# Optimization experiments

Hardware: AMD Instinct MI355X
Metric: run time of the kernel (lower is better)

The kernel has to match this reference:

```python
import jax, jax.numpy as jnp
import numpy as np

J, F_ = 17, 32  # joints x per-joint features; C = J*F_ = 544
H = 8           # num_heads
EPS = 1e-5


def _layernorm(x, g, b):
    mu = jnp.mean(x, axis=-1, keepdims=True)
    var = jnp.mean((x - mu) ** 2, axis=-1, keepdims=True)
    return (x - mu) * jax.lax.rsqrt(var + EPS) * g + b


def setup_inputs() -> dict:
    key = jax.random.key(0)
    ks = jax.random.split(key, 8)
    B, N, C = 8, 1024, J * F_
    x = jax.random.normal(ks[0], (B, N, C), dtype=jnp.float32)
    s = 1.0 / np.sqrt(C)
    return {
        "x": x,
        "norm_g": jnp.ones((F_,), jnp.float32),
        "norm_b": jnp.zeros((F_,), jnp.float32),
        "ap_w": jax.random.normal(ks[1], (1, F_), jnp.float32) / np.sqrt(F_),
        "ap_b": jnp.zeros((1,), jnp.float32),
        "norm2_g": jnp.ones((C,), jnp.float32),
        "norm2_b": jnp.zeros((C,), jnp.float32),
        "qkv_w": jax.random.normal(ks[2], (3 * C, C), jnp.float32) * s,
        "proj_w": jax.random.normal(ks[3], (C, C), jnp.float32) * s,
        "proj_b": jnp.zeros((C,), jnp.float32),
        "scaling_factor": jnp.array([2.0], jnp.float32),
    }


def reference(x, norm_g, norm_b, ap_w, ap_b, norm2_g, norm2_b, qkv_w, proj_w, proj_b, scaling_factor):
    B, N, C = x.shape
    hd = C // H
    # --- attention pooling over joints ---
    xr = x.reshape(B, N, J, F_)
    xr = _layernorm(xr, norm_g, norm_b)                      # [B,N,17,32]
    scores = jnp.einsum('bnjf,of->bnjo', xr, ap_w)[..., 0] + ap_b[0]  # [B,N,17]
    # nn.Softmax(dim=1): softmax over sequence axis N (faithful to source)
    w = jax.nn.softmax(scores, axis=1)
    xp = (xr * w[..., None]).reshape(B, N, C)
    xp = _layernorm(xp, norm2_g, norm2_b)
    # --- position-scaled self-attention ---
    positions = jnp.linspace(0.0, 1.0, N, dtype=jnp.float32)  # [N]
    pos_scale = jnp.exp(-scaling_factor[0] * (positions - 0.5) ** 2)  # per-key scale
    qkv = (xp @ qkv_w.T).reshape(B, N, 3, H, hd)
    q = qkv[:, :, 0].transpose(0, 2, 1, 3)  # [B,H,N,hd]
    k = qkv[:, :, 1].transpose(0, 2, 1, 3)
    v = qkv[:, :, 2].transpose(0, 2, 1, 3)
    scale = hd ** -0.5
    attn = jnp.einsum('bhqd,bhkd->bhqk', q, k) * (scale * pos_scale[None, None, None, :])
    attn = jax.nn.softmax(attn, axis=-1)
    out = jnp.einsum('bhqk,bhkd->bhqd', attn, v)
    out = out.transpose(0, 2, 1, 3).reshape(B, N, C)
    return out @ proj_w.T + proj_b
```

## Files before the change

kernel.cpp:

```cpp
#include <hip/hip_runtime.h>
#include <hip/hip_bf16.h>

#define BB 8
#define NN 1024
#define CC 544
#define JJ 17
#define FF 32
#define HH 8
#define HD 68
#define BN 8192
#define KD 544
#define NCQ 1632
#define NCQP 1664
#define NCPP 640
#define NKB 9
#define BHSZ 73728
#define AQR 64

using f32x4  = __attribute__((ext_vector_type(4))) float;
using bf16x8 = __attribute__((ext_vector_type(8))) short;

__device__ __forceinline__ void gld_lds16(const void* g, void* l) {
  __builtin_amdgcn_global_load_lds(
      (const __attribute__((address_space(1))) void*)g,
      (__attribute__((address_space(3))) void*)l, 16, 0, 0);
}

__global__ __launch_bounds__(256) void wconv(const float* __restrict__ qkv_w,
                                             const float* __restrict__ proj_w,
                                             __hip_bfloat16* __restrict__ qw,
                                             __hip_bfloat16* __restrict__ pw,
                                             char* __restrict__ qkp) {
  int bid = blockIdx.x, t = threadIdx.x;
  if (bid < NCQP + NCPP) {
    bool isq = bid < NCQP;
    int r = isq ? bid : bid - NCQP;
    const float* src = isq ? qkv_w : proj_w;
    __hip_bfloat16* dst = isq ? qw : pw;
    int nrows = isq ? NCQ : CC;
    if (t < KD / 4) {
      int c = t * 4;
      float4 v;
      if (r < nrows) v = *(const float4*)(src + (size_t)r * KD + c);
      else           v = float4{0.f, 0.f, 0.f, 0.f};
      __hip_bfloat16 o[4] = {__float2bfloat16(v.x), __float2bfloat16(v.y),
                             __float2bfloat16(v.z), __float2bfloat16(v.w)};
      *(unsigned long long*)(dst + (size_t)r * KD + c) = *(unsigned long long*)o;
    }
  } else {
    int row = (bid - (NCQP + NCPP)) * 256 + t;
    if (row < 131072) {
      int bhT = row >> 10, n = row & 1023;
      char* p = qkp + (size_t)bhT * 147456 + 131072 + (size_t)n * 16 + 8;
      *(unsigned long long*)p = 0ull;
    }
  }
}

__global__ __launch_bounds__(256) void ln1_scores(const float* __restrict__ x,
                                                  const float* __restrict__ g,
                                                  const float* __restrict__ bta,
                                                  const float* __restrict__ apw,
                                                  const float* __restrict__ apb,
                                                  __hip_bfloat16* __restrict__ xr,
                                                  float* __restrict__ scores) {
  int wv = threadIdx.x >> 6, lane = threadIdx.x & 63;
  int bn = blockIdx.x * 4 + wv;
  int f = lane & 31, half = lane >> 5;
  const float* row = x + (size_t)bn * CC;
  float gg = g[f], bb = bta[f], aw = apw[f], ab = apb[0];
  for (int it = 0; it < 9; ++it) {
    int j = it * 2 + half;
    bool act = (j < JJ);
    float v = act ? row[j * FF + f] : 0.f;
    float s = v;
    for (int m = 16; m >= 1; m >>= 1) s += __shfl_xor(s, m);
    float mu = s * (1.f / 32.f);
    float dv = v - mu;
    float s2 = dv * dv;
    for (int m = 16; m >= 1; m >>= 1) s2 += __shfl_xor(s2, m);
    float xn = dv * rsqrtf(s2 * (1.f / 32.f) + 1e-5f) * gg + bb;
    float sc = xn * aw;
    for (int m = 16; m >= 1; m >>= 1) sc += __shfl_xor(sc, m);
    if (act) {
      xr[(size_t)bn * CC + j * FF + f] = __float2bfloat16(xn);
      if (f == 0) scores[bn * JJ + j] = sc + ab;
    }
  }
}

__global__ __launch_bounds__(256) void softmax_red(const float* __restrict__ scores,
                                                   float2* __restrict__ tab) {
  int bj = blockIdx.x;
  int b = bj / JJ, j = bj - b * JJ;
  const float* s = scores + (size_t)b * NN * JJ + j;
  int t = threadIdx.x;
  float v[4];
  float mx = -1e30f;
#pragma unroll
  for (int i = 0; i < 4; ++i) { v[i] = s[(t + 256 * i) * JJ]; mx = fmaxf(mx, v[i]); }
#pragma unroll
  for (int m = 32; m >= 1; m >>= 1) mx = fmaxf(mx, __shfl_xor(mx, m));
  __shared__ float red[4];
  if ((t & 63) == 0) red[t >> 6] = mx;
  __syncthreads();
  mx = fmaxf(fmaxf(red[0], red[1]), fmaxf(red[2], red[3]));
  float sum = 0.f;
#pragma unroll
  for (int i = 0; i < 4; ++i) sum += __expf(v[i] - mx);
#pragma unroll
  for (int m = 32; m >= 1; m >>= 1) sum += __shfl_xor(sum, m);
  __shared__ float red2[4];
  if ((t & 63) == 0) red2[t >> 6] = sum;
  __syncthreads();
  if (t == 0) {
    sum = red2[0] + red2[1] + red2[2] + red2[3];
    tab[bj] = make_float2(mx, 1.f / sum);
  }
}

__global__ __launch_bounds__(256) void ln2_xp(const __hip_bfloat16* __restrict__ xr,
                                              const float* __restrict__ scores,
                                              const float2* __restrict__ tab,
                                              const float* __restrict__ g2,
                                              const float* __restrict__ b2,
                                              __hip_bfloat16* __restrict__ xp) {
  __shared__ float wsh[4][JJ];
  int wv = threadIdx.x >> 6, lane = threadIdx.x & 63;
  int bn = blockIdx.x * 4 + wv;
  if (lane < JJ) {
    float sc = scores[bn * JJ + lane];
    float2 mi = tab[(bn >> 10) * JJ + lane];
    wsh[wv][lane] = __expf(sc - mi.x) * mi.y;
  }
  float vals[9];
  float sum = 0.f;
  for (int it = 0; it < 9; ++it) {
    int c = it * 64 + lane;
    float v = 0.f;
    if (c < CC) v = __bfloat162float(xr[(size_t)bn * CC + c]) * wsh[wv][c >> 5];
    vals[it] = v;
    sum += v;
  }
  for (int m = 32; m >= 1; m >>= 1) sum += __shfl_xor(sum, m);
  float mu = sum * (1.f / 544.f);
  float s2 = 0.f;
  for (int it = 0; it < 9; ++it) {
    int c = it * 64 + lane;
    if (c < CC) { float dv = vals[it] - mu; s2 += dv * dv; }
  }
  for (int m = 32; m >= 1; m >>= 1) s2 += __shfl_xor(s2, m);
  float rstd = rsqrtf(s2 * (1.f / 544.f) + 1e-5f);
  for (int it = 0; it < 9; ++it) {
    int c = it * 64 + lane;
    if (c < CC)
      xp[(size_t)bn * CC + c] = __float2bfloat16((vals[it] - mu) * rstd * g2[c] + b2[c]);
  }
}

template <int MODE>
__global__ __launch_bounds__(256) void gemm_nt(const __hip_bfloat16* __restrict__ A,
                                               const __hip_bfloat16* __restrict__ Bw,
                                               __hip_bfloat16* __restrict__ Qp,
                                               __hip_bfloat16* __restrict__ Kp,
                                               __hip_bfloat16* __restrict__ Vt,
                                               float* __restrict__ Cf,
                                               const float* __restrict__ bias,
                                               const float* __restrict__ sfp) {
  __shared__ __hip_bfloat16 As[2][128 * 32];
  __shared__ __hip_bfloat16 Bs[2][128 * 32];
  const int t = threadIdx.x;
  const int w = t >> 6, lane = t & 63;
  const int fr = lane & 15, fq = lane >> 4;
  const int bi = blockIdx.x;
  const int xcd = bi & 7, j = bi >> 3;
  const int bx = xcd * 8 + (j & 7), by = j >> 3;
  const int m0 = bx * 128;
  const int n0 = by * 128;
  const int wm = (w >> 1) * 64, wn = (w & 1) * 64;

  f32x4 acc[4][4] = {};

  const __hip_bfloat16* Ag = A + (size_t)m0 * KD;
  const __hip_bfloat16* Bg = Bw + (size_t)n0 * KD;

#pragma unroll
  for (int i2 = 0; i2 < 2; ++i2) {
    int cb = (i2 * 4 + w) * 64;
    int chunk = cb + lane;
    int row = chunk >> 2, c16 = chunk & 3;
    gld_lds16(Ag + (size_t)row * KD + c16 * 8, &As[0][cb * 8]);
    gld_lds16(Bg + (size_t)row * KD + c16 * 8, &Bs[0][cb * 8]);
  }
  __syncthreads();

  for (int kt = 0; kt < 17; ++kt) {
    const int cur = kt & 1;
    if (kt < 16) {
      const int k0 = (kt + 1) * 32;
#pragma unroll
      for (int i2 = 0; i2 < 2; ++i2) {
        int cb = (i2 * 4 + w) * 64;
        int chunk = cb + lane;
        int row = chunk >> 2, c16 = chunk & 3;
        gld_lds16(Ag + (size_t)row * KD + k0 + c16 * 8, &As[1 - cur][cb * 8]);
        gld_lds16(Bg + (size_t)row * KD + k0 + c16 * 8, &Bs[1 - cur][cb * 8]);
      }
    }
    bf16x8 af[4], bfr[4];
#pragma unroll
    for (int tm = 0; tm < 4; ++tm)
      af[tm] = *(const bf16x8*)&As[cur][(wm + tm * 16 + fr) * 32 + fq * 8];
#pragma unroll
    for (int tn = 0; tn < 4; ++tn)
      bfr[tn] = *(const bf16x8*)&Bs[cur][(wn + tn * 16 + fr) * 32 + fq * 8];
#pragma unroll
    for (int tm = 0; tm < 4; ++tm)
#pragma unroll
      for (int tn = 0; tn < 4; ++tn)
        acc[tm][tn] = __builtin_amdgcn_mfma_f32_16x16x32_bf16(af[tm], bfr[tn], acc[tm][tn], 0, 0, 0);
    __syncthreads();
  }

  if (MODE == 1) {
#pragma unroll
    for (int tn = 0; tn < 4; ++tn) {
      int o = n0 + wn + tn * 16 + fr;
      if (o < CC) {
        float bb = bias[o];
#pragma unroll
        for (int tm = 0; tm < 4; ++tm) {
          int m = m0 + wm + tm * 16 + fq * 4;
#pragma unroll
          for (int r = 0; r < 4; ++r)
            Cf[(size_t)(m + r) * CC + o] = acc[tm][tn][r] + bb;
        }
      }
    }
  } else {
    int b = m0 >> 10;
    float sf = sfp[0];
#pragma unroll
    for (int tn = 0; tn < 4; ++tn) {
      int o = n0 + wn + tn * 16 + fr;
      if (o < 2 * CC) {
        bool is_k = (o >= CC);
        int oo = is_k ? o - CC : o;
        int h = oo / HD;
        int d = oo - h * HD;
        __hip_bfloat16* base = is_k ? Kp : Qp;
        __hip_bfloat16* dst = base + (size_t)(b * HH + h) * BHSZ + (d >> 3) * (NN * 8) + (d & 7);
#pragma unroll
        for (int tm = 0; tm < 4; ++tm) {
          int m = m0 + wm + tm * 16 + fq * 4;
          int n = m & (NN - 1);
#pragma unroll
          for (int r = 0; r < 4; ++r) {
            float v = acc[tm][tn][r];
            if (is_k) {
              float pos = (n + r) * (1.f / 1023.f) - 0.5f;
              v *= __expf(-sf * pos * pos) * (0.12126781251816650f * 1.44269504088896340f);
            }
            dst[(size_t)(n + r) * 8] = __float2bfloat16(v);
          }
        }
      } else if (o < NCQ) {
        int oo = o - 2 * CC;
        int h = oo / HD;
        int d = oo - h * HD;
        __hip_bfloat16* vrow = Vt + (((size_t)b * HH + h) * HD + d) * NN;
#pragma unroll
        for (int tm = 0; tm < 4; ++tm) {
          int m = m0 + wm + tm * 16 + fq * 4;
          int n = m & (NN - 1);
#pragma unroll
          for (int r = 0; r < 4; ++r)
            vrow[n + r] = __float2bfloat16(acc[tm][tn][r]);
        }
      }
    }
  }
}

__global__ __launch_bounds__(128) void attn_kernel(const __hip_bfloat16* __restrict__ Qp,
                                                   const __hip_bfloat16* __restrict__ Kp,
                                                   const __hip_bfloat16* __restrict__ Vt,
                                                   __hip_bfloat16* __restrict__ Ao) {
  __shared__ __hip_bfloat16 Qs[NKB * 64 * 8];
  __shared__ __hip_bfloat16 Ks[2][NKB * 64 * 8];
  __shared__ __hip_bfloat16 Zs[64 * 8];
  const int t = threadIdx.x;
  const int w = t >> 6, lane = t & 63;
  const int fr = lane & 15, fq = lane >> 4;
  const int idx = blockIdx.x;
  const int bh = idx & 63, qt = idx >> 6;
  const int h = bh & 7, b = bh >> 3;

  const __hip_bfloat16* qtile = Qp + (size_t)bh * BHSZ + (size_t)qt * AQR * 8;
  const __hip_bfloat16* kbase = Kp + (size_t)bh * BHSZ;
  const __hip_bfloat16* vbase = Vt + (size_t)bh * HD * NN;

  *(unsigned long long*)&Zs[t * 4] = 0ull;
#pragma unroll
  for (int i = 0; i < 5; ++i) {
    int kb = i * 2 + w;
    if (kb < NKB) gld_lds16(qtile + (size_t)kb * (NN * 8) + lane * 8, &Qs[kb * 64 * 8]);
  }
#pragma unroll
  for (int i = 0; i < 5; ++i) {
    int kb = i * 2 + w;
    if (kb < NKB) gld_lds16(kbase + (size_t)kb * (NN * 8) + lane * 8, &Ks[0][kb * 64 * 8]);
  }
  __syncthreads();
  bf16x8 qa[2][3];
#pragma unroll
  for (int ks = 0; ks < 3; ++ks) {
    const __hip_bfloat16* qb = (ks < 2 || fq == 0) ? &Qs[(ks * 4 + fq) * 64 * 8] : Zs;
#pragma unroll
    for (int g = 0; g < 2; ++g)
      qa[g][ks] = *(const bf16x8*)&qb[(w * 32 + g * 16 + fr) * 8];
  }
  __syncthreads();

  f32x4 o_acc[2][5] = {};
  float l_part[2][4] = {};
  const int dclamp = (fr < 4) ? 0 : 1;

  for (int kt = 0; kt < 16; ++kt) {
    const int cur = kt & 1;
    bf16x8 vfrag[5][2];
#pragma unroll
    for (int tv = 0; tv < 5; ++tv) {
      int d = tv * 16 + fr;
      int dc = (tv == 4 && dclamp) ? 0 : d;
#pragma unroll
      for (int ks2 = 0; ks2 < 2; ++ks2)
        vfrag[tv][ks2] = *(const bf16x8*)(vbase + (size_t)dc * NN + kt * 64 + ks2 * 32 + fq * 8);
    }
    if (kt < 15) {
      const __hip_bfloat16* ktile = kbase + (size_t)(kt + 1) * 64 * 8;
#pragma unroll
      for (int i = 0; i < 5; ++i) {
        int kb = i * 2 + w;
        if (kb < NKB) gld_lds16(ktile + (size_t)kb * (NN * 8) + lane * 8, &Ks[1 - cur][kb * 64 * 8]);
      }
    }

    f32x4 s[2][4] = {};
#pragma unroll
    for (int ks = 0; ks < 3; ++ks) {
      const __hip_bfloat16* kbL = (ks < 2 || fq == 0) ? &Ks[cur][(ks * 4 + fq) * 64 * 8] : Zs;
#pragma unroll
      for (int tn = 0; tn < 4; ++tn) {
        bf16x8 kb = *(const bf16x8*)&kbL[(tn * 16 + fr) * 8];
        s[0][tn] = __builtin_amdgcn_mfma_f32_16x16x32_bf16(qa[0][ks], kb, s[0][tn], 0, 0, 0);
        s[1][tn] = __builtin_amdgcn_mfma_f32_16x16x32_bf16(qa[1][ks], kb, s[1][tn], 0, 0, 0);
      }
    }
#pragma unroll
    for (int g = 0; g < 2; ++g) {
      __hip_bfloat16* Pw = &Qs[(w * 2 + g) * 1152];
#pragma unroll
      for (int tn = 0; tn < 4; ++tn)
#pragma unroll
        for (int r = 0; r < 4; ++r) {
          float p = __builtin_amdgcn_exp2f(s[g][tn][r]);
          l_part[g][r] += p;
          Pw[(fq * 4 + r) * 72 + tn * 16 + fr] = __float2bfloat16(p);
        }
    }
#pragma unroll
    for (int ks2 = 0; ks2 < 2; ++ks2) {
      bf16x8 pa0 = *(const bf16x8*)&Qs[(w * 2 + 0) * 1152 + fr * 72 + ks2 * 32 + fq * 8];
      bf16x8 pa1 = *(const bf16x8*)&Qs[(w * 2 + 1) * 1152 + fr * 72 + ks2 * 32 + fq * 8];
#pragma unroll
      for (int tv = 0; tv < 5; ++tv) {
        o_acc[0][tv] = __builtin_amdgcn_mfma_f32_16x16x32_bf16(pa0, vfrag[tv][ks2], o_acc[0][tv], 0, 0, 0);
        o_acc[1][tv] = __builtin_amdgcn_mfma_f32_16x16x32_bf16(pa1, vfrag[tv][ks2], o_acc[1][tv], 0, 0, 0);
      }
    }
    __syncthreads();
  }
#pragma unroll
  for (int g = 0; g < 2; ++g) {
    __hip_bfloat16* obase = Ao + (size_t)(b * NN + qt * AQR + w * 32 + g * 16) * CC + h * HD;
    float inv[4];
#pragma unroll
    for (int r = 0; r < 4; ++r) {
      float l = l_part[g][r];
#pragma unroll
      for (int msk = 8; msk >= 1; msk >>= 1) l += __shfl_xor(l, msk);
      inv[r] = 1.f / l;
    }
#pragma unroll
    for (int tv = 0; tv < 5; ++tv) {
      int d = tv * 16 + fr;
      if (d < HD) {
#pragma unroll
        for (int r = 0; r < 4; ++r)
          obase[(size_t)(fq * 4 + r) * CC + d] = __float2bfloat16(o_acc[g][tv][r] * inv[r]);
      }
    }
  }
}

extern "C" void kernel_launch(void* const* d_in, const int* in_sizes, int n_in,
                              void* d_out, int out_size, void* d_ws, size_t ws_size,
                              hipStream_t stream) {
  (void)in_sizes; (void)n_in; (void)out_size; (void)ws_size;
  const float* x       = (const float*)d_in[0];
  const float* norm_g  = (const float*)d_in[1];
  const float* norm_b  = (const float*)d_in[2];
  const float* ap_w    = (const float*)d_in[3];
  const float* ap_b    = (const float*)d_in[4];
  const float* norm2_g = (const float*)d_in[5];
  const float* norm2_b = (const float*)d_in[6];
  const float* qkv_w   = (const float*)d_in[7];
  const float* proj_w  = (const float*)d_in[8];
  const float* proj_b  = (const float*)d_in[9];
  const float* sf      = (const float*)d_in[10];
  float* out = (float*)d_out;
  char* ws = (char*)d_ws;

  __hip_bfloat16* xr   = (__hip_bfloat16*)(ws);
  float* scores        = (float*)(ws + 8912896);
  float2* tab          = (float2*)(ws + 9469952);
  __hip_bfloat16* xp   = (__hip_bfloat16*)(ws + 9474048);
  __hip_bfloat16* qw   = (__hip_bfloat16*)(ws + 18386944);
  __hip_bfloat16* pw   = (__hip_bfloat16*)(ws + 20197376);
  __hip_bfloat16* vt   = (__hip_bfloat16*)(ws + 20893696);
  __hip_bfloat16* ao   = (__hip_bfloat16*)(ws + 29806592);
  __hip_bfloat16* qp   = (__hip_bfloat16*)(ws + 38719488);
  __hip_bfloat16* kp   = (__hip_bfloat16*)(ws + 48156672);

  wconv<<<NCQP + NCPP + 512, 256, 0, stream>>>(qkv_w, proj_w, qw, pw, (char*)qp);
  ln1_scores<<<BN / 4, 256, 0, stream>>>(x, norm_g, norm_b, ap_w, ap_b, xr, scores);
  softmax_red<<<BB * JJ, 256, 0, stream>>>(scores, tab);
  ln2_xp<<<BN / 4, 256, 0, stream>>>(xr, scores, tab, norm2_g, norm2_b, xp);
  gemm_nt<0><<<dim3(64 * 13), 256, 0, stream>>>(xp, qw, qp, kp, vt, nullptr, nullptr, sf);
  attn_kernel<<<dim3((NN / AQR) * HH * BB), 128, 0, stream>>>(qp, kp, vt, ao);
  gemm_nt<1><<<dim3(64 * 5), 256, 0, stream>>>(ao, pw, nullptr, nullptr, nullptr, out, proj_b, nullptr);
}
```

Measured before the change: 218.5 us.

## Split attention key range across two wave pairs with LDS reduction

Attention blocks go from 128 to 256 threads. Two wave pairs each handle half of the key tiles (split-K), and their partial outputs and row sums are combined through shared memory at the end. This doubles the waves working per query tile, which should hide latency better on a grid of 1024 blocks. In exchange it drops the K double-buffer prefetch: each iteration now loads K and then synchronises. It also adds a cross-wave reduction and raises LDS use per block.

```diff
diff --git a/kernel.cpp b/kernel.cpp
--- a/kernel.cpp
+++ b/kernel.cpp
@@ -282,15 +282,17 @@
   }
 }
 
-__global__ __launch_bounds__(128) void attn_kernel(const __hip_bfloat16* __restrict__ Qp,
+__global__ __launch_bounds__(256) void attn_kernel(const __hip_bfloat16* __restrict__ Qp,
                                                    const __hip_bfloat16* __restrict__ Kp,
                                                    const __hip_bfloat16* __restrict__ Vt,
                                                    __hip_bfloat16* __restrict__ Ao) {
   __shared__ __hip_bfloat16 Qs[NKB * 64 * 8];
+  __shared__ __hip_bfloat16 Ps1[NKB * 64 * 8];
   __shared__ __hip_bfloat16 Ks[2][NKB * 64 * 8];
   __shared__ __hip_bfloat16 Zs[64 * 8];
   const int t = threadIdx.x;
   const int w = t >> 6, lane = t & 63;
+  const int p = w >> 1, wv = w & 1;
   const int fr = lane & 15, fq = lane >> 4;
   const int idx = blockIdx.x;
   const int bh = idx & 63, qt = idx >> 6;
@@ -300,34 +302,39 @@
   const __hip_bfloat16* kbase = Kp + (size_t)bh * BHSZ;
   const __hip_bfloat16* vbase = Vt + (size_t)bh * HD * NN;
 
-  *(unsigned long long*)&Zs[t * 4] = 0ull;
-#pragma unroll
-  for (int i = 0; i < 5; ++i) {
-    int kb = i * 2 + w;
-    if (kb < NKB) gld_lds16(qtile + (size_t)kb * (NN * 8) + lane * 8, &Qs[kb * 64 * 8]);
-  }
-#pragma unroll
-  for (int i = 0; i < 5; ++i) {
-    int kb = i * 2 + w;
-    if (kb < NKB) gld_lds16(kbase + (size_t)kb * (NN * 8) + lane * 8, &Ks[0][kb * 64 * 8]);
+  if (t < 128) *(unsigned long long*)&Zs[t * 4] = 0ull;
+#pragma unroll
+  for (int i = 0; i < 3; ++i) {
+    int kb = i * 4 + w;
+    if (kb < NKB) gld_lds16(qtile + (size_t)kb * (NN * 8) + lane * 8, &Qs[kb * 512]);
   }
   __syncthreads();
   bf16x8 qa[2][3];
 #pragma unroll
   for (int ks = 0; ks < 3; ++ks) {
-    const __hip_bfloat16* qb = (ks < 2 || fq == 0) ? &Qs[(ks * 4 + fq) * 64 * 8] : Zs;
+    const __hip_bfloat16* qb = (ks < 2 || fq == 0) ? &Qs[(ks * 4 + fq) * 512] : Zs;
 #pragma unroll
     for (int g = 0; g < 2; ++g)
-      qa[g][ks] = *(const bf16x8*)&qb[(w * 32 + g * 16 + fr) * 8];
+      qa[g][ks] = *(const bf16x8*)&qb[(wv * 32 + g * 16 + fr) * 8];
   }
   __syncthreads();
+
+  __hip_bfloat16* Pbase = (p == 0) ? Qs : Ps1;
 
   f32x4 o_acc[2][5] = {};
   float l_part[2][4] = {};
   const int dclamp = (fr < 4) ? 0 : 1;
 
-  for (int kt = 0; kt < 16; ++kt) {
-    const int cur = kt & 1;
+  for (int kt8 = 0; kt8 < 8; ++kt8) {
+    const int ktg = p * 8 + kt8;
+    const __hip_bfloat16* ktile = kbase + (size_t)ktg * 64 * 8;
+#pragma unroll
+    for (int i = 0; i < 5; ++i) {
+      int kb = i * 2 + wv;
+      if (kb < NKB) gld_lds16(ktile + (size_t)kb * (NN * 8) + lane * 8, &Ks[p][kb * 512]);
+    }
+    __syncthreads();
+
     bf16x8 vfrag[5][2];
 #pragma unroll
     for (int tv = 0; tv < 5; ++tv) {
@@ -335,21 +342,13 @@
       int dc = (tv == 4 && dclamp) ? 0 : d;
 #pragma unroll
       for (int ks2 = 0; ks2 < 2; ++ks2)
-        vfrag[tv][ks2] = *(const bf16x8*)(vbase + (size_t)dc * NN + kt * 64 + ks2 * 32 + fq * 8);
-    }
-    if (kt < 15) {
-      const __hip_bfloat16* ktile = kbase + (size_t)(kt + 1) * 64 * 8;
-#pragma unroll
-      for (int i = 0; i < 5; ++i) {
-        int kb = i * 2 + w;
-        if (kb < NKB) gld_lds16(ktile + (size_t)kb * (NN * 8) + lane * 8, &Ks[1 - cur][kb * 64 * 8]);
-      }
+        vfrag[tv][ks2] = *(const bf16x8*)(vbase + (size_t)dc * NN + ktg * 64 + ks2 * 32 + fq * 8);
     }
 
     f32x4 s[2][4] = {};
 #pragma unroll
     for (int ks = 0; ks < 3; ++ks) {
-      const __hip_bfloat16* kbL = (ks < 2 || fq == 0) ? &Ks[cur][(ks * 4 + fq) * 64 * 8] : Zs;
+      const __hip_bfloat16* kbL = (ks < 2 || fq == 0) ? &Ks[p][(ks * 4 + fq) * 512] : Zs;
 #pragma unroll
       for (int tn = 0; tn < 4; ++tn) {
         bf16x8 kb = *(const bf16x8*)&kbL[(tn * 16 + fr) * 8];
@@ -359,20 +358,20 @@
     }
 #pragma unroll
     for (int g = 0; g < 2; ++g) {
-      __hip_bfloat16* Pw = &Qs[(w * 2 + g) * 1152];
+      __hip_bfloat16* Pw = &Pbase[(wv * 2 + g) * 1152];
 #pragma unroll
       for (int tn = 0; tn < 4; ++tn)
 #pragma unroll
         for (int r = 0; r < 4; ++r) {
-          float p = __builtin_amdgcn_exp2f(s[g][tn][r]);
-          l_part[g][r] += p;
-          Pw[(fq * 4 + r) * 72 + tn * 16 + fr] = __float2bfloat16(p);
+          float pe = __builtin_amdgcn_exp2f(s[g][tn][r]);
+          l_part[g][r] += pe;
+          Pw[(fq * 4 + r) * 72 + tn * 16 + fr] = __float2bfloat16(pe);
         }
     }
 #pragma unroll
     for (int ks2 = 0; ks2 < 2; ++ks2) {
-      bf16x8 pa0 = *(const bf16x8*)&Qs[(w * 2 + 0) * 1152 + fr * 72 + ks2 * 32 + fq * 8];
-      bf16x8 pa1 = *(const bf16x8*)&Qs[(w * 2 + 1) * 1152 + fr * 72 + ks2 * 32 + fq * 8];
+      bf16x8 pa0 = *(const bf16x8*)&Pbase[(wv * 2 + 0) * 1152 + fr * 72 + ks2 * 32 + fq * 8];
+      bf16x8 pa1 = *(const bf16x8*)&Pbase[(wv * 2 + 1) * 1152 + fr * 72 + ks2 * 32 + fq * 8];
 #pragma unroll
       for (int tv = 0; tv < 5; ++tv) {
         o_acc[0][tv] = __builtin_amdgcn_mfma_f32_16x16x32_bf16(pa0, vfrag[tv][ks2], o_acc[0][tv], 0, 0, 0);
@@ -381,24 +380,54 @@
     }
     __syncthreads();
   }
+
+  float* xb = (float*)Ks;
 #pragma unroll
   for (int g = 0; g < 2; ++g) {
-    __hip_bfloat16* obase = Ao + (size_t)(b * NN + qt * AQR + w * 32 + g * 16) * CC + h * HD;
-    float inv[4];
-#pragma unroll
-    for (int r = 0; r < 4; ++r) {
-      float l = l_part[g][r];
-#pragma unroll
-      for (int msk = 8; msk >= 1; msk >>= 1) l += __shfl_xor(l, msk);
-      inv[r] = 1.f / l;
-    }
-#pragma unroll
-    for (int tv = 0; tv < 5; ++tv) {
-      int d = tv * 16 + fr;
-      if (d < HD) {
-#pragma unroll
-        for (int r = 0; r < 4; ++r)
-          obase[(size_t)(fq * 4 + r) * CC + d] = __float2bfloat16(o_acc[g][tv][r] * inv[r]);
+    if (p == 1) {
+#pragma unroll
+      for (int tv = 0; tv < 5; ++tv)
+#pragma unroll
+        for (int i = 0; i < 4; ++i)
+          xb[(wv * 24 + tv * 4 + i) * 64 + lane] = o_acc[g][tv][i];
+#pragma unroll
+      for (int r = 0; r < 4; ++r)
+        xb[(wv * 24 + 20 + r) * 64 + lane] = l_part[g][r];
+    }
+    __syncthreads();
+    if (p == 0) {
+#pragma unroll
+      for (int tv = 0; tv < 5; ++tv)
+#pragma unroll
+        for (int i = 0; i < 4; ++i)
+          o_acc[g][tv][i] += xb[(wv * 24 + tv * 4 + i) * 64 + lane];
+#pragma unroll
+      for (int r = 0; r < 4; ++r)
+        l_part[g][r] += xb[(wv * 24 + 20 + r) * 64 + lane];
+    }
+    __syncthreads();
+  }
+
+  if (p == 0) {
+#pragma unroll
+    for (int g = 0; g < 2; ++g) {
+      __hip_bfloat16* obase = Ao + (size_t)(b * NN + qt * AQR + wv * 32 + g * 16) * CC + h * HD;
+      float inv[4];
+#pragma unroll
+      for (int r = 0; r < 4; ++r) {
+        float l = l_part[g][r];
+#pragma unroll
+        for (int msk = 8; msk >= 1; msk >>= 1) l += __shfl_xor(l, msk);
+        inv[r] = 1.f / l;
+      }
+#pragma unroll
+      for (int tv = 0; tv < 5; ++tv) {
+        int d = tv * 16 + fr;
+        if (d < HD) {
+#pragma unroll
+          for (int r = 0; r < 4; ++r)
+            obase[(size_t)(fq * 4 + r) * CC + d] = __float2bfloat16(o_acc[g][tv][r] * inv[r]);
+        }
       }
     }
   }
@@ -438,6 +467,6 @@
   softmax_red<<<BB * JJ, 256, 0, stream>>>(scores, tab);
   ln2_xp<<<BN / 4, 256, 0, stream>>>(xr, scores, tab, norm2_g, norm2_b, xp);
   gemm_nt<0><<<dim3(64 * 13), 256, 0, stream>>>(xp, qw, qp, kp, vt, nullptr, nullptr, sf);
-  attn_kernel<<<dim3((NN / AQR) * HH * BB), 128, 0, stream>>>(qp, kp, vt, ao);
+  attn_kernel<<<dim3((NN / AQR) * HH * BB), 256, 0, stream>>>(qp, kp, vt, ao);
   gemm_nt<1><<<dim3(64 * 5), 256, 0, stream>>>(ao, pw, nullptr, nullptr, nullptr, out, proj_b, nullptr);
 }
```

Measured after the change: 222.6 us. No clear change (+1.9%).

## Use explicit vmcnt waits and setprio to overlap K prefetch in attention

Applied to the files above, without the earlier changes.

Each wave now issues all 9 K/Q async global-to-LDS loads itself instead of splitting them across the two waves. __syncthreads is replaced by explicit s_waitcnt vmcnt counters plus s_barrier, so the next K tile's prefetch stays in flight while the current tile is consumed. MFMA sections are wrapped with s_setprio to favour matrix work. The aim is to hide load latency and cut barrier stalls, but the hand-counted vmcnt values are fragile and each wave now issues twice as many loads.

```diff
diff --git a/kernel.cpp b/kernel.cpp
--- a/kernel.cpp
+++ b/kernel.cpp
@@ -302,25 +302,27 @@
 
   *(unsigned long long*)&Zs[t * 4] = 0ull;
 #pragma unroll
-  for (int i = 0; i < 5; ++i) {
-    int kb = i * 2 + w;
-    if (kb < NKB) gld_lds16(qtile + (size_t)kb * (NN * 8) + lane * 8, &Qs[kb * 64 * 8]);
-  }
-#pragma unroll
-  for (int i = 0; i < 5; ++i) {
-    int kb = i * 2 + w;
-    if (kb < NKB) gld_lds16(kbase + (size_t)kb * (NN * 8) + lane * 8, &Ks[0][kb * 64 * 8]);
-  }
-  __syncthreads();
+  for (int kb = 0; kb < NKB; ++kb)
+    gld_lds16(qtile + (size_t)kb * (NN * 8) + lane * 8, &Qs[kb * 512]);
+#pragma unroll
+  for (int kb = 0; kb < NKB; ++kb)
+    gld_lds16(kbase + (size_t)kb * (NN * 8) + lane * 8, &Ks[0][kb * 512]);
+  asm volatile("s_waitcnt vmcnt(9)" ::: "memory");
+  __builtin_amdgcn_sched_barrier(0);
+  asm volatile("s_waitcnt lgkmcnt(0)" ::: "memory");
+  __builtin_amdgcn_sched_barrier(0);
+  __builtin_amdgcn_s_barrier();
   bf16x8 qa[2][3];
 #pragma unroll
   for (int ks = 0; ks < 3; ++ks) {
-    const __hip_bfloat16* qb = (ks < 2 || fq == 0) ? &Qs[(ks * 4 + fq) * 64 * 8] : Zs;
+    const __hip_bfloat16* qb = (ks < 2 || fq == 0) ? &Qs[(ks * 4 + fq) * 512] : Zs;
 #pragma unroll
     for (int g = 0; g < 2; ++g)
       qa[g][ks] = *(const bf16x8*)&qb[(w * 32 + g * 16 + fr) * 8];
   }
-  __syncthreads();
+  asm volatile("s_waitcnt lgkmcnt(0)" ::: "memory");
+  __builtin_amdgcn_sched_barrier(0);
+  __builtin_amdgcn_s_barrier();
 
   f32x4 o_acc[2][5] = {};
   float l_part[2][4] = {};
@@ -337,19 +339,23 @@
       for (int ks2 = 0; ks2 < 2; ++ks2)
         vfrag[tv][ks2] = *(const bf16x8*)(vbase + (size_t)dc * NN + kt * 64 + ks2 * 32 + fq * 8);
     }
+    __builtin_amdgcn_sched_barrier(0);
     if (kt < 15) {
       const __hip_bfloat16* ktile = kbase + (size_t)(kt + 1) * 64 * 8;
 #pragma unroll
-      for (int i = 0; i < 5; ++i) {
-        int kb = i * 2 + w;
-        if (kb < NKB) gld_lds16(ktile + (size_t)kb * (NN * 8) + lane * 8, &Ks[1 - cur][kb * 64 * 8]);
-      }
-    }
+      for (int kb = 0; kb < NKB; ++kb)
+        gld_lds16(ktile + (size_t)kb * (NN * 8) + lane * 8, &Ks[1 - cur][kb * 512]);
+      asm volatile("s_waitcnt vmcnt(19)" ::: "memory");
+    } else {
+      asm volatile("s_waitcnt vmcnt(10)" ::: "memory");
+    }
+    __builtin_amdgcn_sched_barrier(0);
 
     f32x4 s[2][4] = {};
+    __builtin_amdgcn_s_setprio(1);
 #pragma unroll
     for (int ks = 0; ks < 3; ++ks) {
-      const __hip_bfloat16* kbL = (ks < 2 || fq == 0) ? &Ks[cur][(ks * 4 + fq) * 64 * 8] : Zs;
+      const __hip_bfloat16* kbL = (ks < 2 || fq == 0) ? &Ks[cur][(ks * 4 + fq) * 512] : Zs;
 #pragma unroll
       for (int tn = 0; tn < 4; ++tn) {
         bf16x8 kb = *(const bf16x8*)&kbL[(tn * 16 + fr) * 8];
@@ -357,6 +363,7 @@
         s[1][tn] = __builtin_amdgcn_mfma_f32_16x16x32_bf16(qa[1][ks], kb, s[1][tn], 0, 0, 0);
       }
     }
+    __builtin_amdgcn_s_setprio(0);
 #pragma unroll
     for (int g = 0; g < 2; ++g) {
       __hip_bfloat16* Pw = &Qs[(w * 2 + g) * 1152];
@@ -364,11 +371,12 @@
       for (int tn = 0; tn < 4; ++tn)
 #pragma unroll
         for (int r = 0; r < 4; ++r) {
-          float p = __builtin_amdgcn_exp2f(s[g][tn][r]);
-          l_part[g][r] += p;
-          Pw[(fq * 4 + r) * 72 + tn * 16 + fr] = __float2bfloat16(p);
+          float pe = __builtin_amdgcn_exp2f(s[g][tn][r]);
+          l_part[g][r] += pe;
+          Pw[(fq * 4 + r) * 72 + tn * 16 + fr] = __float2bfloat16(pe);
         }
     }
+    __builtin_amdgcn_s_setprio(1);
 #pragma unroll
     for (int ks2 = 0; ks2 < 2; ++ks2) {
       bf16x8 pa0 = *(const bf16x8*)&Qs[(w * 2 + 0) * 1152 + fr * 72 + ks2 * 32 + fq * 8];
@@ -379,7 +387,10 @@
         o_acc[1][tv] = __builtin_amdgcn_mfma_f32_16x16x32_bf16(pa1, vfrag[tv][ks2], o_acc[1][tv], 0, 0, 0);
       }
     }
-    __syncthreads();
+    __builtin_amdgcn_s_setprio(0);
+    asm volatile("s_waitcnt lgkmcnt(0)" ::: "memory");
+    __builtin_amdgcn_sched_barrier(0);
+    __builtin_amdgcn_s_barrier();
   }
 #pragma unroll
   for (int g = 0; g < 2; ++g) {
```

After: 251.3 us. +15.0%, slower.

## Load Q and K fragments directly from global into registers, drop LDS staging

Applied to the files above, without the earlier changes.

The attention kernel stops staging Q and K tiles in shared memory through async global-to-LDS copies with double buffering. Each lane now loads its MFMA fragments straight from global memory into registers and zeroes the padded head-dim block with a select. Shared memory shrinks to a per-wave P buffer, and the per-iteration block barrier is removed because each wave only touches its own P region. The cost is redundant global/L2 reads of K (each wave loads the same K tile), no prefetch overlap, and more register pressure.

```diff
diff --git a/kernel.cpp b/kernel.cpp
--- a/kernel.cpp
+++ b/kernel.cpp
@@ -282,13 +282,11 @@
   }
 }
 
-__global__ __launch_bounds__(128) void attn_kernel(const __hip_bfloat16* __restrict__ Qp,
-                                                   const __hip_bfloat16* __restrict__ Kp,
-                                                   const __hip_bfloat16* __restrict__ Vt,
-                                                   __hip_bfloat16* __restrict__ Ao) {
-  __shared__ __hip_bfloat16 Qs[NKB * 64 * 8];
-  __shared__ __hip_bfloat16 Ks[2][NKB * 64 * 8];
-  __shared__ __hip_bfloat16 Zs[64 * 8];
+__global__ __launch_bounds__(128, 1) void attn_kernel(const __hip_bfloat16* __restrict__ Qp,
+                                                      const __hip_bfloat16* __restrict__ Kp,
+                                                      const __hip_bfloat16* __restrict__ Vt,
+                                                      __hip_bfloat16* __restrict__ Ao) {
+  __shared__ __hip_bfloat16 Ps[4 * 1152];
   const int t = threadIdx.x;
   const int w = t >> 6, lane = t & 63;
   const int fr = lane & 15, fq = lane >> 4;
@@ -296,38 +294,44 @@
   const int bh = idx & 63, qt = idx >> 6;
   const int h = bh & 7, b = bh >> 3;
 
-  const __hip_bfloat16* qtile = Qp + (size_t)bh * BHSZ + (size_t)qt * AQR * 8;
+  const __hip_bfloat16* qbase = Qp + (size_t)bh * BHSZ;
   const __hip_bfloat16* kbase = Kp + (size_t)bh * BHSZ;
   const __hip_bfloat16* vbase = Vt + (size_t)bh * HD * NN;
 
-  *(unsigned long long*)&Zs[t * 4] = 0ull;
-#pragma unroll
-  for (int i = 0; i < 5; ++i) {
-    int kb = i * 2 + w;
-    if (kb < NKB) gld_lds16(qtile + (size_t)kb * (NN * 8) + lane * 8, &Qs[kb * 64 * 8]);
-  }
-#pragma unroll
-  for (int i = 0; i < 5; ++i) {
-    int kb = i * 2 + w;
-    if (kb < NKB) gld_lds16(kbase + (size_t)kb * (NN * 8) + lane * 8, &Ks[0][kb * 64 * 8]);
-  }
-  __syncthreads();
+  const bf16x8 zero8 = {};
+
   bf16x8 qa[2][3];
 #pragma unroll
   for (int ks = 0; ks < 3; ++ks) {
-    const __hip_bfloat16* qb = (ks < 2 || fq == 0) ? &Qs[(ks * 4 + fq) * 64 * 8] : Zs;
-#pragma unroll
-    for (int g = 0; g < 2; ++g)
-      qa[g][ks] = *(const bf16x8*)&qb[(w * 32 + g * 16 + fr) * 8];
-  }
-  __syncthreads();
+    int kblk = ks * 4 + fq;
+    int kbc = kblk > 8 ? 8 : kblk;
+#pragma unroll
+    for (int g = 0; g < 2; ++g) {
+      bf16x8 v = *(const bf16x8*)(qbase + (size_t)kbc * (NN * 8) +
+                                  ((size_t)qt * AQR + w * 32 + g * 16 + fr) * 8);
+      if (kblk > 8) v = zero8;
+      qa[g][ks] = v;
+    }
+  }
 
   f32x4 o_acc[2][5] = {};
   float l_part[2][4] = {};
   const int dclamp = (fr < 4) ? 0 : 1;
 
   for (int kt = 0; kt < 16; ++kt) {
-    const int cur = kt & 1;
+    bf16x8 kf[3][4];
+#pragma unroll
+    for (int ks = 0; ks < 3; ++ks) {
+      int kblk = ks * 4 + fq;
+      int kbc = kblk > 8 ? 8 : kblk;
+      const __hip_bfloat16* kp0 = kbase + (size_t)kbc * (NN * 8) + ((size_t)kt * 64 + fr) * 8;
+#pragma unroll
+      for (int tn = 0; tn < 4; ++tn) {
+        bf16x8 v = *(const bf16x8*)(kp0 + tn * 128);
+        if (kblk > 8) v = zero8;
+        kf[ks][tn] = v;
+      }
+    }
     bf16x8 vfrag[5][2];
 #pragma unroll
     for (int tv = 0; tv < 5; ++tv) {
@@ -337,49 +341,37 @@
       for (int ks2 = 0; ks2 < 2; ++ks2)
         vfrag[tv][ks2] = *(const bf16x8*)(vbase + (size_t)dc * NN + kt * 64 + ks2 * 32 + fq * 8);
     }
-    if (kt < 15) {
-      const __hip_bfloat16* ktile = kbase + (size_t)(kt + 1) * 64 * 8;
-#pragma unroll
-      for (int i = 0; i < 5; ++i) {
-        int kb = i * 2 + w;
-        if (kb < NKB) gld_lds16(ktile + (size_t)kb * (NN * 8) + lane * 8, &Ks[1 - cur][kb * 64 * 8]);
-      }
-    }
 
     f32x4 s[2][4] = {};
 #pragma unroll
-    for (int ks = 0; ks < 3; ++ks) {
-      const __hip_bfloat16* kbL = (ks < 2 || fq == 0) ? &Ks[cur][(ks * 4 + fq) * 64 * 8] : Zs;
+    for (int ks = 0; ks < 3; ++ks)
 #pragma unroll
       for (int tn = 0; tn < 4; ++tn) {
-        bf16x8 kb = *(const bf16x8*)&kbL[(tn * 16 + fr) * 8];
-        s[0][tn] = __builtin_amdgcn_mfma_f32_16x16x32_bf16(qa[0][ks], kb, s[0][tn], 0, 0, 0);
-        s[1][tn] = __builtin_amdgcn_mfma_f32_16x16x32_bf16(qa[1][ks], kb, s[1][tn], 0, 0, 0);
-      }
-    }
+        s[0][tn] = __builtin_amdgcn_mfma_f32_16x16x32_bf16(qa[0][ks], kf[ks][tn], s[0][tn], 0, 0, 0);
+        s[1][tn] = __builtin_amdgcn_mfma_f32_16x16x32_bf16(qa[1][ks], kf[ks][tn], s[1][tn], 0, 0, 0);
+      }
 #pragma unroll
     for (int g = 0; g < 2; ++g) {
-      __hip_bfloat16* Pw = &Qs[(w * 2 + g) * 1152];
+      __hip_bfloat16* Pw = &Ps[(w * 2 + g) * 1152];
 #pragma unroll
       for (int tn = 0; tn < 4; ++tn)
 #pragma unroll
         for (int r = 0; r < 4; ++r) {
-          float p = __builtin_amdgcn_exp2f(s[g][tn][r]);
-          l_part[g][r] += p;
-          Pw[(fq * 4 + r) * 72 + tn * 16 + fr] = __float2bfloat16(p);
+          float pe = __builtin_amdgcn_exp2f(s[g][tn][r]);
+          l_part[g][r] += pe;
+          Pw[(fq * 4 + r) * 72 + tn * 16 + fr] = __float2bfloat16(pe);
         }
     }
 #pragma unroll
     for (int ks2 = 0; ks2 < 2; ++ks2) {
-      bf16x8 pa0 = *(const bf16x8*)&Qs[(w * 2 + 0) * 1152 + fr * 72 + ks2 * 32 + fq * 8];
-      bf16x8 pa1 = *(const bf16x8*)&Qs[(w * 2 + 1) * 1152 + fr * 72 + ks2 * 32 + fq * 8];
+      bf16x8 pa0 = *(const bf16x8*)&Ps[(w * 2 + 0) * 1152 + fr * 72 + ks2 * 32 + fq * 8];
+      bf16x8 pa1 = *(const bf16x8*)&Ps[(w * 2 + 1) * 1152 + fr * 72 + ks2 * 32 + fq * 8];
 #pragma unroll
       for (int tv = 0; tv < 5; ++tv) {
         o_acc[0][tv] = __builtin_amdgcn_mfma_f32_16x16x32_bf16(pa0, vfrag[tv][ks2], o_acc[0][tv], 0, 0, 0);
         o_acc[1][tv] = __builtin_amdgcn_mfma_f32_16x16x32_bf16(pa1, vfrag[tv][ks2], o_acc[1][tv], 0, 0, 0);
       }
     }
-    __syncthreads();
   }
 #pragma unroll
   for (int g = 0; g < 2; ++g) {
```

New measurement: 226.7 us. 3.8% more time.
